# Kernel optimization log

Measured on AMD Instinct MI355X. Metric: run time of the kernel, lower is better.

Reference implementation:

```python
import jax, jax.numpy as jnp
import numpy as np

B = 4
T, Hh, Ww = 16, 32, 32
C = 256
HEADS = 8
WIN = 4
SHIFT = 2
MLP = 1024


def _rel_pos_index(w):
    coords = np.stack(np.meshgrid(np.arange(w), np.arange(w), np.arange(w), indexing='ij')).reshape(3, -1)
    rc = (coords[:, :, None] - coords[:, None, :]).transpose(1, 2, 0)
    rc[:, :, 0] += w - 1
    rc[:, :, 1] += w - 1
    rc[:, :, 2] += w - 1
    rc[:, :, 0] *= (2 * w - 1) * (2 * w - 1)
    rc[:, :, 1] *= 2 * w - 1
    return rc.sum(-1).astype(np.int32)  # (w^3, w^3)


def _attn_mask(t, h, w, win, shift):
    m = np.zeros((t, h, w))
    sl = (slice(0, -win), slice(-win, -shift), slice(-shift, None))
    cnt = 0
    for a in sl:
        for b in sl:
            for c in sl:
                m[a, b, c] = cnt
                cnt += 1
    m = m.reshape(t // win, win, h // win, win, w // win, win).transpose(0, 2, 4, 1, 3, 5).reshape(-1, win ** 3)
    am = m[:, None, :] - m[:, :, None]  # (nW, N, N)
    return np.where(am != 0, -100.0, 0.0).astype(np.float32)


def setup_inputs() -> dict:
    key = jax.random.key(0)
    ks = jax.random.split(key, 12)
    s_in = 1.0 / np.sqrt(C)
    s_mlp = 1.0 / np.sqrt(MLP)
    return {
        'x': jax.random.normal(ks[0], (B, T * Hh * Ww, C), jnp.float32),
        'norm1_g': jnp.ones((C,), jnp.float32),
        'norm1_b': jnp.zeros((C,), jnp.float32),
        'qkv_w': jax.random.normal(ks[1], (C, 3 * C), jnp.float32) * s_in,
        'qkv_b': jax.random.normal(ks[2], (3 * C,), jnp.float32) * 0.02,
        'proj_w': jax.random.normal(ks[3], (C, C), jnp.float32) * s_in,
        'proj_b': jax.random.normal(ks[4], (C,), jnp.float32) * 0.02,
        'rel_bias_table': jax.random.normal(ks[5], ((2 * WIN - 1) ** 3, HEADS), jnp.float32) * 0.02,
        'norm2_g': jnp.ones((C,), jnp.float32),
        'norm2_b': jnp.zeros((C,), jnp.float32),
        'mlp_w1': jax.random.normal(ks[6], (C, MLP), jnp.float32) * s_in,
        'mlp_b1': jax.random.normal(ks[7], (MLP,), jnp.float32) * 0.02,
        'mlp_w2': jax.random.normal(ks[8], (MLP, C), jnp.float32) * s_mlp,
        'mlp_b2': jax.random.normal(ks[9], (C,), jnp.float32) * 0.02,
        'rel_index': jnp.asarray(_rel_pos_index(WIN)),
        'attn_mask': jnp.asarray(_attn_mask(T, Hh, Ww, WIN, SHIFT)),
    }


def _ln(x, g, b, eps):
    mu = x.mean(-1, keepdims=True)
    var = ((x - mu) ** 2).mean(-1, keepdims=True)
    return (x - mu) * jax.lax.rsqrt(var + eps) * g + b


def reference(x, norm1_g, norm1_b, qkv_w, qkv_b, proj_w, proj_b, rel_bias_table,
              norm2_g, norm2_b, mlp_w1, mlp_b1, mlp_w2, mlp_b2, rel_index, attn_mask):
    w = WIN
    N = w ** 3
    hd = C // HEADS
    scale = hd ** -0.5

    h = _ln(x, norm1_g, norm1_b, 1e-5).reshape(B, T, Hh, Ww, C)
    h = jnp.roll(h, shift=(-SHIFT, -SHIFT, -SHIFT), axis=(1, 2, 3))
    # window partition -> (B*nW, N, C)
    h = h.reshape(B, T // w, w, Hh // w, w, Ww // w, w, C)
    h = h.transpose(0, 1, 3, 5, 2, 4, 6, 7).reshape(-1, N, C)

    qkv = (h @ qkv_w + qkv_b).reshape(-1, N, 3, HEADS, hd)
    qkv = qkv.transpose(2, 0, 3, 1, 4)  # (3, BW, heads, N, hd)
    q, k, v = qkv[0] * scale, qkv[1], qkv[2]
    attn = jnp.einsum('bhid,bhjd->bhij', q, k)

    bias = rel_bias_table[rel_index.reshape(-1)].reshape(N, N, HEADS).transpose(2, 0, 1)
    attn = attn + bias[None]

    nW = attn_mask.shape[0]
    attn = attn.reshape(-1, nW, HEADS, N, N) + attn_mask[None, :, None]
    attn = jax.nn.softmax(attn.reshape(-1, HEADS, N, N), axis=-1)

    o = jnp.einsum('bhij,bhjd->bhid', attn, v).transpose(0, 2, 1, 3).reshape(-1, N, C)
    o = o @ proj_w + proj_b
    # window reverse
    o = o.reshape(B, T // w, Hh // w, Ww // w, w, w, w, C)
    o = o.transpose(0, 1, 4, 2, 5, 3, 6, 7).reshape(B, T, Hh, Ww, C)
    o = jnp.roll(o, shift=(SHIFT, SHIFT, SHIFT), axis=(1, 2, 3)).reshape(B, T * Hh * Ww, C)

    x = x + o
    y = _ln(x, norm2_g, norm2_b, 1e-6)
    y = jax.nn.gelu(y @ mlp_w1 + mlp_b1, approximate=False) @ mlp_w2 + mlp_b2
    return x + y
```

## Files before the change

kernel.cpp:

```cpp
#include <hip/hip_runtime.h>
#include <cstdint>
#include <cstddef>

typedef float  f32x4_t  __attribute__((ext_vector_type(4)));
typedef __bf16 bf16x8_t __attribute__((ext_vector_type(8)));
typedef __bf16 bf16x4_t __attribute__((ext_vector_type(4)));

#define NTOK   65536
#define CCH    256
#define NWINT  1024

__device__ __forceinline__ float wred_sum(float v) {
#pragma unroll
  for (int off = 32; off > 0; off >>= 1) v += __shfl_xor(v, off, 64);
  return v;
}

__device__ __forceinline__ void gload16(void* lds, const void* g) {
  __builtin_amdgcn_global_load_lds(
      (const __attribute__((address_space(1))) uint32_t*)g,
      (__attribute__((address_space(3))) uint32_t*)lds, 16, 0, 0);
}

__device__ __forceinline__ int win_to_orig(int token) {
  int gid = token >> 6, n = token & 63;
  int bb = gid >> 8, rem = gid & 255;
  int t = (((rem >> 6) << 2) + (n >> 4) + 2) & 15;
  int h = ((((rem >> 3) & 7) << 2) + ((n >> 2) & 3) + 2) & 31;
  int w = (((rem & 7) << 2) + (n & 3) + 2) & 31;
  return ((bb * 16 + t) * 32 + h) * 32 + w;
}

__global__ __launch_bounds__(256) void prep_weights(
    const float* __restrict__ qkv_w, const float* __restrict__ proj_w,
    const float* __restrict__ mlp_w1, const float* __restrict__ mlp_w2,
    __bf16* __restrict__ wt_qkv, __bf16* __restrict__ wt_proj,
    __bf16* __restrict__ wt_mlp1, __bf16* __restrict__ wt_mlp2) {
  int i = blockIdx.x * 256 + threadIdx.x;
  if (i < 196608) {
    int k = i / 768, n = i % 768;
    wt_qkv[n * 256 + k] = (__bf16)qkv_w[i];
  } else if (i < 262144) {
    int j = i - 196608;
    int k = j >> 8, n = j & 255;
    wt_proj[n * 256 + k] = (__bf16)proj_w[j];
  } else if (i < 524288) {
    int j = i - 262144;
    int k = j >> 10, n = j & 1023;
    wt_mlp1[n * 256 + k] = (__bf16)mlp_w1[j];
  } else {
    int j = i - 524288;
    int k = j >> 8, n = j & 255;
    wt_mlp2[n * 1024 + k] = (__bf16)mlp_w2[j];
  }
}

__global__ __launch_bounds__(256) void cm_prep(
    const float* __restrict__ table, const int* __restrict__ ridx,
    const float* __restrict__ mask, __bf16* __restrict__ cm) {
  int tid = blockIdx.x * 256 + threadIdx.x;
  int l = tid & 63;
  int t16 = (tid >> 6) & 15;
  int h = (tid >> 10) & 7;
  int w = tid >> 13;
  int it = t16 & 3, jt = t16 >> 2;
  int i = it * 16 + (l & 15);
  int jb = jt * 16 + ((l >> 4) << 2);
  const float* mrow = mask + (size_t)w * 4096 + i * 64;
  const int* rrow = ridx + i * 64;
  bf16x4_t o;
#pragma unroll
  for (int r = 0; r < 4; ++r) {
    int j = jb + r;
    o[r] = (__bf16)(table[rrow[j] * 8 + h] + mrow[j]);
  }
  *(bf16x4_t*)(cm + (size_t)tid * 4) = o;
}

template <int MODE>
__global__ __launch_bounds__(256) void ln_kernel(
    const float* __restrict__ xin, const float* __restrict__ g,
    const float* __restrict__ b, __bf16* __restrict__ out, float eps) {
  int token = blockIdx.x * 4 + (threadIdx.x >> 6);
  int lane = threadIdx.x & 63;
  size_t src = (MODE == 0) ? (size_t)win_to_orig(token) : (size_t)token;
  f32x4_t v = ((const f32x4_t*)(xin + src * CCH))[lane];
  float mu = wred_sum(v[0] + v[1] + v[2] + v[3]) * (1.0f / 256.0f);
  float d0 = v[0] - mu, d1 = v[1] - mu, d2 = v[2] - mu, d3 = v[3] - mu;
  float var = wred_sum(d0 * d0 + d1 * d1 + d2 * d2 + d3 * d3) * (1.0f / 256.0f);
  float rs = rsqrtf(var + eps);
  f32x4_t gg = ((const f32x4_t*)g)[lane];
  f32x4_t bb = ((const f32x4_t*)b)[lane];
  bf16x4_t o;
  o[0] = (__bf16)(d0 * rs * gg[0] + bb[0]);
  o[1] = (__bf16)(d1 * rs * gg[1] + bb[1]);
  o[2] = (__bf16)(d2 * rs * gg[2] + bb[2]);
  o[3] = (__bf16)(d3 * rs * gg[3] + bb[3]);
  *(bf16x4_t*)(out + (size_t)token * CCH + lane * 4) = o;
}

#define BM 128
#define BN 128
#define BK 64
template <int EPI>
__global__ __launch_bounds__(256) void gemm_kernel(
    const __bf16* __restrict__ A, const __bf16* __restrict__ Bt,
    const float* __restrict__ bias, const float* __restrict__ res,
    void* __restrict__ outp, int M, int N, int K) {
  __shared__ bf16x8_t smA[1024];
  __shared__ bf16x8_t smB[1024];
  const int wv = threadIdx.x >> 6;
  const int ln = threadIdx.x & 63;
  const int bm = blockIdx.y * BM;
  const int bn = blockIdx.x * BN;
  const int wr = wv >> 1, wc = wv & 1;

  f32x4_t acc[4][4];
#pragma unroll
  for (int m = 0; m < 4; ++m)
#pragma unroll
    for (int n = 0; n < 4; ++n) acc[m][n] = (f32x4_t){0.f, 0.f, 0.f, 0.f};

  const int KT = K >> 6;
  for (int kt = 0; kt < KT; ++kt) {
#pragma unroll
    for (int it = 0; it < 4; ++it) {
      int base = (it * 4 + wv) * 64;
      int slot = base + ln;
      int row = slot >> 3;
      int chunk = (slot & 7) ^ (row & 7);
      gload16((void*)(smA + base),
              (const void*)(A + (size_t)(bm + row) * K + kt * BK + chunk * 8));
      gload16((void*)(smB + base),
              (const void*)(Bt + (size_t)(bn + row) * K + kt * BK + chunk * 8));
    }
    __syncthreads();

#pragma unroll
    for (int kh = 0; kh < 2; ++kh) {
      bf16x8_t af[4], bfr[4];
#pragma unroll
      for (int m = 0; m < 4; ++m) {
        int row = wr * 64 + m * 16 + (ln & 15);
        int c = (kh * 4 + (ln >> 4)) ^ (row & 7);
        af[m] = *(const bf16x8_t*)((const char*)smA + row * 128 + c * 16);
      }
#pragma unroll
      for (int n = 0; n < 4; ++n) {
        int row = wc * 64 + n * 16 + (ln & 15);
        int c = (kh * 4 + (ln >> 4)) ^ (row & 7);
        bfr[n] = *(const bf16x8_t*)((const char*)smB + row * 128 + c * 16);
      }
#pragma unroll
      for (int m = 0; m < 4; ++m)
#pragma unroll
        for (int n = 0; n < 4; ++n)
          acc[m][n] = __builtin_amdgcn_mfma_f32_16x16x32_bf16(
              af[m], bfr[n], acc[m][n], 0, 0, 0);
    }
    __syncthreads();
  }

#pragma unroll
  for (int m = 0; m < 4; ++m) {
    int grow0 = bm + wr * 64 + m * 16 + ((ln >> 4) * 4);
#pragma unroll
    for (int n = 0; n < 4; ++n) {
      int gcol = bn + wc * 64 + n * 16 + (ln & 15);
      float bv = bias[gcol];
#pragma unroll
      for (int r = 0; r < 4; ++r) {
        int grow = grow0 + r;
        float v = acc[m][n][r] + bv;
        if constexpr (EPI == 0) {
          ((__bf16*)outp)[(size_t)grow * N + gcol] = (__bf16)v;
        } else if constexpr (EPI == 1) {
          size_t dst = (size_t)win_to_orig(grow) * CCH + gcol;
          ((float*)outp)[dst] = res[dst] + v;
        } else if constexpr (EPI == 2) {
          float gl = 0.5f * v * (1.0f + erff(v * 0.70710678118654752f));
          ((__bf16*)outp)[(size_t)grow * N + gcol] = (__bf16)gl;
        } else {
          size_t o = (size_t)grow * N + gcol;
          ((float*)outp)[o] = res[o] + v;
        }
      }
    }
  }
}

__global__ __launch_bounds__(256) void attn_mfma(
    const __bf16* __restrict__ qkv, const __bf16* __restrict__ cm,
    __bf16* __restrict__ owin) {
  __shared__ __align__(16) __bf16 smP[4][64 * 72];
  __shared__ __align__(16) __bf16 smV[4][64 * 32];
  const int wv = threadIdx.x >> 6;
  const int ln = threadIdx.x & 63;
  const int task = blockIdx.x * 4 + wv;
  const int win = task >> 3;
  const int h = task & 7;
  const int i15 = ln & 15, g = ln >> 4;

  const __bf16* base = qkv + (size_t)win * 64 * 768 + h * 32;

  {
    __bf16* vdst = smV[wv];
#pragma unroll
    for (int c = 0; c < 4; ++c) {
      const __bf16* src =
          base + (size_t)(c * 16 + (ln >> 2)) * 768 + 512 + (ln & 3) * 8;
      gload16(vdst + c * 512, src);
    }
  }

  bf16x8_t kf[4], qf[4];
#pragma unroll
  for (int t = 0; t < 4; ++t) {
    kf[t] = *(const bf16x8_t*)(base + (size_t)(t * 16 + i15) * 768 + 256 + g * 8);
    qf[t] = *(const bf16x8_t*)(base + (size_t)(t * 16 + i15) * 768 + g * 8);
  }

  f32x4_t st[4][4];
#pragma unroll
  for (int jt = 0; jt < 4; ++jt)
#pragma unroll
    for (int it = 0; it < 4; ++it)
      st[jt][it] = __builtin_amdgcn_mfma_f32_16x16x32_bf16(
          kf[jt], qf[it], (f32x4_t){0.f, 0.f, 0.f, 0.f}, 0, 0, 0);

  const __bf16* cmp = cm + (((size_t)(win & 255) * 8 + h) * 16) * 256;
#pragma unroll
  for (int jt = 0; jt < 4; ++jt)
#pragma unroll
    for (int it = 0; it < 4; ++it) {
      bf16x4_t c4 = *(const bf16x4_t*)(cmp + ((jt * 4 + it) * 64 + ln) * 4);
#pragma unroll
      for (int r = 0; r < 4; ++r)
        st[jt][it][r] =
            fmaf(st[jt][it][r], 0.17677669529663687f, (float)c4[r]);
    }

#pragma unroll
  for (int it = 0; it < 4; ++it) {
    float mx = -1e30f;
#pragma unroll
    for (int jt = 0; jt < 4; ++jt)
#pragma unroll
      for (int r = 0; r < 4; ++r) mx = fmaxf(mx, st[jt][it][r]);
    mx = fmaxf(mx, __shfl_xor(mx, 16, 64));
    mx = fmaxf(mx, __shfl_xor(mx, 32, 64));
    float sum = 0.f;
#pragma unroll
    for (int jt = 0; jt < 4; ++jt)
#pragma unroll
      for (int r = 0; r < 4; ++r) {
        float p = __expf(st[jt][it][r] - mx);
        st[jt][it][r] = p;
        sum += p;
      }
    sum += __shfl_xor(sum, 16, 64);
    sum += __shfl_xor(sum, 32, 64);
    float inv = 1.0f / sum;
#pragma unroll
    for (int jt = 0; jt < 4; ++jt) {
      bf16x4_t p4;
#pragma unroll
      for (int r = 0; r < 4; ++r) p4[r] = (__bf16)(st[jt][it][r] * inv);
      *(bf16x4_t*)(smP[wv] + (it * 16 + i15) * 72 + jt * 16 + g * 4) = p4;
    }
  }
  __syncthreads();

  f32x4_t oacc[4][2];
#pragma unroll
  for (int it = 0; it < 4; ++it)
#pragma unroll
    for (int dt = 0; dt < 2; ++dt) oacc[it][dt] = (f32x4_t){0.f, 0.f, 0.f, 0.f};

  const __bf16* pl = smP[wv];
  const __bf16* vl = smV[wv];
#pragma unroll
  for (int kt = 0; kt < 2; ++kt) {
    bf16x8_t vf[2];
#pragma unroll
    for (int dt = 0; dt < 2; ++dt)
#pragma unroll
      for (int e = 0; e < 8; ++e)
        vf[dt][e] = vl[(kt * 32 + g * 8 + e) * 32 + dt * 16 + i15];
#pragma unroll
    for (int it = 0; it < 4; ++it) {
      bf16x8_t pa =
          *(const bf16x8_t*)(pl + (it * 16 + i15) * 72 + kt * 32 + g * 8);
#pragma unroll
      for (int dt = 0; dt < 2; ++dt)
        oacc[it][dt] = __builtin_amdgcn_mfma_f32_16x16x32_bf16(
            pa, vf[dt], oacc[it][dt], 0, 0, 0);
    }
  }

  __bf16* op = owin + (size_t)win * 64 * 256 + h * 32;
#pragma unroll
  for (int it = 0; it < 4; ++it)
#pragma unroll
    for (int r = 0; r < 4; ++r) {
      int i = it * 16 + g * 4 + r;
#pragma unroll
      for (int dt = 0; dt < 2; ++dt)
        op[(size_t)i * 256 + dt * 16 + i15] = (__bf16)oacc[it][dt][r];
    }
}

extern "C" void kernel_launch(void* const* d_in, const int* in_sizes, int n_in,
                              void* d_out, int out_size, void* d_ws,
                              size_t ws_size, hipStream_t stream) {
  (void)in_sizes; (void)n_in; (void)out_size; (void)ws_size;
  const float* x      = (const float*)d_in[0];
  const float* n1g    = (const float*)d_in[1];
  const float* n1b    = (const float*)d_in[2];
  const float* qkv_w  = (const float*)d_in[3];
  const float* qkv_b  = (const float*)d_in[4];
  const float* proj_w = (const float*)d_in[5];
  const float* proj_b = (const float*)d_in[6];
  const float* rbt    = (const float*)d_in[7];
  const float* n2g    = (const float*)d_in[8];
  const float* n2b    = (const float*)d_in[9];
  const float* mlp_w1 = (const float*)d_in[10];
  const float* mlp_b1 = (const float*)d_in[11];
  const float* mlp_w2 = (const float*)d_in[12];
  const float* mlp_b2 = (const float*)d_in[13];
  const int*   ridx   = (const int*)d_in[14];
  const float* amask  = (const float*)d_in[15];

  char* ws = (char*)d_ws;
  size_t off = 0;
  auto alloc = [&](size_t bytes) {
    void* p = ws + off;
    off += (bytes + 255) & ~(size_t)255;
    return p;
  };
  __bf16* wt_qkv  = (__bf16*)alloc(768 * 256 * 2);
  __bf16* wt_proj = (__bf16*)alloc(256 * 256 * 2);
  __bf16* wt_mlp1 = (__bf16*)alloc(1024 * 256 * 2);
  __bf16* wt_mlp2 = (__bf16*)alloc(1024 * 256 * 2);
  __bf16* hwin = (__bf16*)alloc((size_t)NTOK * 256 * 2);
  __bf16* qkv  = (__bf16*)alloc((size_t)NTOK * 768 * 2);
  __bf16* owin = (__bf16*)alloc((size_t)NTOK * 256 * 2);
  __bf16* cmb  = hwin;
  __bf16* yb   = hwin;
  __bf16* mlph = qkv;
  float* x2    = (float*)d_out;

  prep_weights<<<3072, 256, 0, stream>>>(qkv_w, proj_w, mlp_w1, mlp_w2,
                                         wt_qkv, wt_proj, wt_mlp1, wt_mlp2);
  ln_kernel<0><<<NTOK / 4, 256, 0, stream>>>(x, n1g, n1b, hwin, 1e-5f);
  gemm_kernel<0><<<dim3(768 / BN, NTOK / BM), 256, 0, stream>>>(
      hwin, wt_qkv, qkv_b, nullptr, qkv, NTOK, 768, 256);
  cm_prep<<<8192, 256, 0, stream>>>(rbt, ridx, amask, cmb);
  attn_mfma<<<2048, 256, 0, stream>>>(qkv, cmb, owin);
  gemm_kernel<1><<<dim3(256 / BN, NTOK / BM), 256, 0, stream>>>(
      owin, wt_proj, proj_b, x, x2, NTOK, 256, 256);
  ln_kernel<1><<<NTOK / 4, 256, 0, stream>>>(x2, n2g, n2b, yb, 1e-6f);
  gemm_kernel<2><<<dim3(1024 / BN, NTOK / BM), 256, 0, stream>>>(
      yb, wt_mlp1, mlp_b1, nullptr, mlph, NTOK, 1024, 256);
  gemm_kernel<3><<<dim3(256 / BN, NTOK / BM), 256, 0, stream>>>(
      mlph, wt_mlp2, mlp_b2, x2, d_out, NTOK, 256, 1024);
}
```

Baseline: 361.9 us.

## Double-buffer GEMM LDS tiles with async prefetch and XCD-aware block remap

The GEMM kernel now keeps two LDS buffers for the A and B tiles. It issues the next k-tile's global-to-LDS loads before computing on the current one, using explicit vmcnt waits and barriers, so memory latency overlaps with MFMA work. The 2D grid becomes 1D, and block ids are remapped round-robin across the 8 XCDs for better L2 locality. Pointer increments replace per-iteration address math, and the epilogue hoists the bias loads and the win_to_orig row mapping. LDS use doubles, which may lower occupancy, and the hand-written waitcnt counts must match the issued loads exactly.

Result: no change. 359.8 us (-0.6%).

```diff
diff --git a/kernel.cpp b/kernel.cpp
--- a/kernel.cpp
+++ b/kernel.cpp
@@ -107,14 +107,30 @@
     const __bf16* __restrict__ A, const __bf16* __restrict__ Bt,
     const float* __restrict__ bias, const float* __restrict__ res,
     void* __restrict__ outp, int M, int N, int K) {
-  __shared__ bf16x8_t smA[1024];
-  __shared__ bf16x8_t smB[1024];
+  __shared__ __bf16 smA[2][8192];
+  __shared__ __bf16 smB[2][8192];
   const int wv = threadIdx.x >> 6;
   const int ln = threadIdx.x & 63;
-  const int bm = blockIdx.y * BM;
-  const int bn = blockIdx.x * BN;
+  const int i15 = ln & 15, g = ln >> 4;
+
+  int nwg = gridDim.x;
+  int wgid = ((int)blockIdx.x & 7) * (nwg >> 3) + ((int)blockIdx.x >> 3);
+  int nx = N >> 7;
+  int bx = wgid % nx, by = wgid / nx;
+  const int bm = by * BM, bn = bx * BN;
   const int wr = wv >> 1, wc = wv & 1;
 
+  const __bf16* aP[4];
+  const __bf16* bP[4];
+#pragma unroll
+  for (int it = 0; it < 4; ++it) {
+    int slot = (it * 4 + wv) * 64 + ln;
+    int row = slot >> 3;
+    int chunk = (slot & 7) ^ (row & 7);
+    aP[it] = A + (size_t)(bm + row) * K + chunk * 8;
+    bP[it] = Bt + (size_t)(bn + row) * K + chunk * 8;
+  }
+
   f32x4_t acc[4][4];
 #pragma unroll
   for (int m = 0; m < 4; ++m)
@@ -122,35 +138,31 @@
     for (int n = 0; n < 4; ++n) acc[m][n] = (f32x4_t){0.f, 0.f, 0.f, 0.f};
 
   const int KT = K >> 6;
-  for (int kt = 0; kt < KT; ++kt) {
+
+  auto stage = [&](int buf) {
 #pragma unroll
     for (int it = 0; it < 4; ++it) {
-      int base = (it * 4 + wv) * 64;
-      int slot = base + ln;
-      int row = slot >> 3;
-      int chunk = (slot & 7) ^ (row & 7);
-      gload16((void*)(smA + base),
-              (const void*)(A + (size_t)(bm + row) * K + kt * BK + chunk * 8));
-      gload16((void*)(smB + base),
-              (const void*)(Bt + (size_t)(bn + row) * K + kt * BK + chunk * 8));
-    }
-    __syncthreads();
-
+      int base = (it * 4 + wv) * 512;
+      gload16(&smA[buf][base], aP[it]);
+      gload16(&smB[buf][base], bP[it]);
+      aP[it] += BK;
+      bP[it] += BK;
+    }
+  };
+
+  auto compute = [&](int buf) {
+    const __bf16* lA = smA[buf];
+    const __bf16* lB = smB[buf];
 #pragma unroll
     for (int kh = 0; kh < 2; ++kh) {
+      int cA = (((kh * 4) + g) ^ (i15 & 7)) * 8;
       bf16x8_t af[4], bfr[4];
 #pragma unroll
-      for (int m = 0; m < 4; ++m) {
-        int row = wr * 64 + m * 16 + (ln & 15);
-        int c = (kh * 4 + (ln >> 4)) ^ (row & 7);
-        af[m] = *(const bf16x8_t*)((const char*)smA + row * 128 + c * 16);
-      }
-#pragma unroll
-      for (int n = 0; n < 4; ++n) {
-        int row = wc * 64 + n * 16 + (ln & 15);
-        int c = (kh * 4 + (ln >> 4)) ^ (row & 7);
-        bfr[n] = *(const bf16x8_t*)((const char*)smB + row * 128 + c * 16);
-      }
+      for (int m = 0; m < 4; ++m)
+        af[m] = *(const bf16x8_t*)(lA + (wr * 64 + m * 16 + i15) * 64 + cA);
+#pragma unroll
+      for (int n = 0; n < 4; ++n)
+        bfr[n] = *(const bf16x8_t*)(lB + (wc * 64 + n * 16 + i15) * 64 + cA);
 #pragma unroll
       for (int m = 0; m < 4; ++m)
 #pragma unroll
@@ -158,30 +170,51 @@
           acc[m][n] = __builtin_amdgcn_mfma_f32_16x16x32_bf16(
               af[m], bfr[n], acc[m][n], 0, 0, 0);
     }
-    __syncthreads();
-  }
-
+  };
+
+  stage(0);
+  for (int kt = 0; kt < KT - 1; ++kt) {
+    stage((kt + 1) & 1);
+    asm volatile("s_waitcnt vmcnt(8)" ::: "memory");
+    __builtin_amdgcn_s_barrier();
+    asm volatile("" ::: "memory");
+    compute(kt & 1);
+    asm volatile("s_waitcnt lgkmcnt(0)" ::: "memory");
+    __builtin_amdgcn_s_barrier();
+  }
+  asm volatile("s_waitcnt vmcnt(0)" ::: "memory");
+  __builtin_amdgcn_s_barrier();
+  asm volatile("" ::: "memory");
+  compute((KT - 1) & 1);
+
+  float bv[4];
+#pragma unroll
+  for (int n = 0; n < 4; ++n) bv[n] = bias[bn + wc * 64 + n * 16 + i15];
 #pragma unroll
   for (int m = 0; m < 4; ++m) {
-    int grow0 = bm + wr * 64 + m * 16 + ((ln >> 4) * 4);
-#pragma unroll
-    for (int n = 0; n < 4; ++n) {
-      int gcol = bn + wc * 64 + n * 16 + (ln & 15);
-      float bv = bias[gcol];
-#pragma unroll
-      for (int r = 0; r < 4; ++r) {
-        int grow = grow0 + r;
-        float v = acc[m][n][r] + bv;
+    int grow0 = bm + wr * 64 + m * 16 + g * 4;
+#pragma unroll
+    for (int r = 0; r < 4; ++r) {
+      int grow = grow0 + r;
+      size_t rowbase;
+      if constexpr (EPI == 1)
+        rowbase = (size_t)win_to_orig(grow) * CCH;
+      else
+        rowbase = (size_t)grow * N;
+#pragma unroll
+      for (int n = 0; n < 4; ++n) {
+        int gcol = bn + wc * 64 + n * 16 + i15;
+        float v = acc[m][n][r] + bv[n];
         if constexpr (EPI == 0) {
-          ((__bf16*)outp)[(size_t)grow * N + gcol] = (__bf16)v;
+          ((__bf16*)outp)[rowbase + gcol] = (__bf16)v;
         } else if constexpr (EPI == 1) {
-          size_t dst = (size_t)win_to_orig(grow) * CCH + gcol;
+          size_t dst = rowbase + gcol;
           ((float*)outp)[dst] = res[dst] + v;
         } else if constexpr (EPI == 2) {
           float gl = 0.5f * v * (1.0f + erff(v * 0.70710678118654752f));
-          ((__bf16*)outp)[(size_t)grow * N + gcol] = (__bf16)gl;
+          ((__bf16*)outp)[rowbase + gcol] = (__bf16)gl;
         } else {
-          size_t o = (size_t)grow * N + gcol;
+          size_t o = rowbase + gcol;
           ((float*)outp)[o] = res[o] + v;
         }
       }
@@ -353,15 +386,15 @@
   prep_weights<<<3072, 256, 0, stream>>>(qkv_w, proj_w, mlp_w1, mlp_w2,
                                          wt_qkv, wt_proj, wt_mlp1, wt_mlp2);
   ln_kernel<0><<<NTOK / 4, 256, 0, stream>>>(x, n1g, n1b, hwin, 1e-5f);
-  gemm_kernel<0><<<dim3(768 / BN, NTOK / BM), 256, 0, stream>>>(
+  gemm_kernel<0><<<(768 / BN) * (NTOK / BM), 256, 0, stream>>>(
       hwin, wt_qkv, qkv_b, nullptr, qkv, NTOK, 768, 256);
   cm_prep<<<8192, 256, 0, stream>>>(rbt, ridx, amask, cmb);
   attn_mfma<<<2048, 256, 0, stream>>>(qkv, cmb, owin);
-  gemm_kernel<1><<<dim3(256 / BN, NTOK / BM), 256, 0, stream>>>(
+  gemm_kernel<1><<<(256 / BN) * (NTOK / BM), 256, 0, stream>>>(
       owin, wt_proj, proj_b, x, x2, NTOK, 256, 256);
   ln_kernel<1><<<NTOK / 4, 256, 0, stream>>>(x2, n2g, n2b, yb, 1e-6f);
-  gemm_kernel<2><<<dim3(1024 / BN, NTOK / BM), 256, 0, stream>>>(
+  gemm_kernel<2><<<(1024 / BN) * (NTOK / BM), 256, 0, stream>>>(
       yb, wt_mlp1, mlp_b1, nullptr, mlph, NTOK, 1024, 256);
-  gemm_kernel<3><<<dim3(256 / BN, NTOK / BM), 256, 0, stream>>>(
+  gemm_kernel<3><<<(256 / BN) * (NTOK / BM), 256, 0, stream>>>(
       mlph, wt_mlp2, mlp_b2, x2, d_out, NTOK, 256, 1024);
 }
```

## Rewrite GEMMs with double-buffered 64x256 tiles and fuse proj with LayerNorm2

Applied to the files above, without the earlier changes.

Replaces the generic 128x128 GEMM with a templated 64x256-tile kernel that double-buffers the K loop in LDS with BK=32, uses workgroup-id swizzling and vectorized epilogue stores. Fuses the projection GEMM, the residual add and the second LayerNorm into one kernel that computes row statistics through LDS, which removes a separate LN pass over x2. Swaps the erf GELU for a tanh-approximation built on exp, which is cheaper but approximate. The MLP stage now stores h1 and yb in original token order instead of window order. Larger tiles and the launch bound of 4 may raise register pressure.

Result: faster. 350.7 us (-3.1%).

```diff
diff --git a/kernel.cpp b/kernel.cpp
--- a/kernel.cpp
+++ b/kernel.cpp
@@ -8,7 +8,6 @@
 
 #define NTOK   65536
 #define CCH    256
-#define NWINT  1024
 
 __device__ __forceinline__ float wred_sum(float v) {
 #pragma unroll
@@ -29,6 +28,12 @@
   int h = ((((rem >> 3) & 7) << 2) + ((n >> 2) & 3) + 2) & 31;
   int w = (((rem & 7) << 2) + (n & 3) + 2) & 31;
   return ((bb * 16 + t) * 32 + h) * 32 + w;
+}
+
+__device__ __forceinline__ float gelu_f(float v) {
+  float u = v * (0.7978845608028654f + 0.03567740814f * v * v);
+  float t = 1.0f - 2.0f / (__expf(2.0f * u) + 1.0f);
+  return 0.5f * v * (1.0f + t);
 }
 
 __global__ __launch_bounds__(256) void prep_weights(
@@ -77,13 +82,12 @@
   *(bf16x4_t*)(cm + (size_t)tid * 4) = o;
 }
 
-template <int MODE>
 __global__ __launch_bounds__(256) void ln_kernel(
     const float* __restrict__ xin, const float* __restrict__ g,
     const float* __restrict__ b, __bf16* __restrict__ out, float eps) {
   int token = blockIdx.x * 4 + (threadIdx.x >> 6);
   int lane = threadIdx.x & 63;
-  size_t src = (MODE == 0) ? (size_t)win_to_orig(token) : (size_t)token;
+  size_t src = (size_t)win_to_orig(token);
   f32x4_t v = ((const f32x4_t*)(xin + src * CCH))[lane];
   float mu = wred_sum(v[0] + v[1] + v[2] + v[3]) * (1.0f / 256.0f);
   float d0 = v[0] - mu, d1 = v[1] - mu, d2 = v[2] - mu, d3 = v[3] - mu;
@@ -99,92 +103,212 @@
   *(bf16x4_t*)(out + (size_t)token * CCH + lane * 4) = o;
 }
 
-#define BM 128
-#define BN 128
-#define BK 64
-template <int EPI>
-__global__ __launch_bounds__(256) void gemm_kernel(
+
+#define GEMM_KLOOP(KT)                                                        \
+  stage(0, 0);                                                                \
+  asm volatile("s_waitcnt vmcnt(0)" ::: "memory");                            \
+  __syncthreads();                                                            \
+  _Pragma("unroll") for (int kt = 0; kt < (KT); ++kt) {                       \
+    const int cur = kt & 1;                                                   \
+    if (kt + 1 < (KT)) stage(cur ^ 1, kt + 1);                                \
+    const __bf16* lA = smA[cur];                                              \
+    const __bf16* lB = smB[cur];                                              \
+    bf16x8_t af[4], wf[4];                                                    \
+    _Pragma("unroll") for (int mm = 0; mm < 4; ++mm)                          \
+        af[mm] = *(const bf16x8_t*)((const char*)lA + (mm * 16 + i15) * 64 +  \
+                                    (((g ^ (i15 & 3))) << 4));                \
+    _Pragma("unroll") for (int nn = 0; nn < 4; ++nn)                          \
+        wf[nn] = *(const bf16x8_t*)((const char*)lB +                         \
+                                    (wv * 64 + nn * 16 + i15) * 64 +          \
+                                    (((g ^ (i15 & 3))) << 4));                \
+    _Pragma("unroll") for (int nn = 0; nn < 4; ++nn)                          \
+        _Pragma("unroll") for (int mm = 0; mm < 4; ++mm)                      \
+            acc[nn][mm] = __builtin_amdgcn_mfma_f32_16x16x32_bf16(            \
+                wf[nn], af[mm], acc[nn][mm], 0, 0, 0);                        \
+    if (kt + 1 < (KT)) {                                                      \
+      asm volatile("s_waitcnt vmcnt(0) lgkmcnt(0)" ::: "memory");             \
+      __syncthreads();                                                        \
+    }                                                                         \
+  }
+
+template <int N, int K, int EPI>
+__global__ __launch_bounds__(256, 4) void gemm_c(
     const __bf16* __restrict__ A, const __bf16* __restrict__ Bt,
     const float* __restrict__ bias, const float* __restrict__ res,
-    void* __restrict__ outp, int M, int N, int K) {
-  __shared__ bf16x8_t smA[1024];
-  __shared__ bf16x8_t smB[1024];
-  const int wv = threadIdx.x >> 6;
-  const int ln = threadIdx.x & 63;
-  const int bm = blockIdx.y * BM;
-  const int bn = blockIdx.x * BN;
-  const int wr = wv >> 1, wc = wv & 1;
+    void* __restrict__ outp) {
+  constexpr int KT = K / 32;
+  constexpr int NX = N / 256;
+  __shared__ __bf16 smA[2][64 * 32];
+  __shared__ __bf16 smB[2][256 * 32];
+  const int tid = threadIdx.x;
+  const int wv = tid >> 6, ln = tid & 63;
+  const int i15 = ln & 15, g = ln >> 4;
+
+  int nwg = gridDim.x;
+  int wgid = ((int)blockIdx.x & 7) * (nwg >> 3) + ((int)blockIdx.x >> 3);
+  const int bx = wgid % NX, by = wgid / NX;
+  const int bm = by * 64, bn = bx * 256;
+
+  const int rowA = tid >> 2, chA = (tid & 3) ^ ((tid >> 2) & 3);
+  const __bf16* aP = A + (size_t)(bm + rowA) * K + chA * 8;
+  const __bf16* bP[4];
+#pragma unroll
+  for (int rnd = 0; rnd < 4; ++rnd) {
+    int slot = rnd * 256 + tid;
+    int row = slot >> 2, ch = (slot & 3) ^ (row & 3);
+    bP[rnd] = Bt + (size_t)(bn + row) * K + ch * 8;
+  }
+
+  auto stage = [&](int buf, int kt) {
+    gload16(&smA[buf][wv * 512], aP + kt * 32);
+#pragma unroll
+    for (int rnd = 0; rnd < 4; ++rnd)
+      gload16(&smB[buf][rnd * 2048 + wv * 512], bP[rnd] + kt * 32);
+  };
 
   f32x4_t acc[4][4];
 #pragma unroll
-  for (int m = 0; m < 4; ++m)
-#pragma unroll
-    for (int n = 0; n < 4; ++n) acc[m][n] = (f32x4_t){0.f, 0.f, 0.f, 0.f};
-
-  const int KT = K >> 6;
-  for (int kt = 0; kt < KT; ++kt) {
-#pragma unroll
-    for (int it = 0; it < 4; ++it) {
-      int base = (it * 4 + wv) * 64;
-      int slot = base + ln;
-      int row = slot >> 3;
-      int chunk = (slot & 7) ^ (row & 7);
-      gload16((void*)(smA + base),
-              (const void*)(A + (size_t)(bm + row) * K + kt * BK + chunk * 8));
-      gload16((void*)(smB + base),
-              (const void*)(Bt + (size_t)(bn + row) * K + kt * BK + chunk * 8));
-    }
-    __syncthreads();
-
-#pragma unroll
-    for (int kh = 0; kh < 2; ++kh) {
-      bf16x8_t af[4], bfr[4];
-#pragma unroll
-      for (int m = 0; m < 4; ++m) {
-        int row = wr * 64 + m * 16 + (ln & 15);
-        int c = (kh * 4 + (ln >> 4)) ^ (row & 7);
-        af[m] = *(const bf16x8_t*)((const char*)smA + row * 128 + c * 16);
+  for (int nn = 0; nn < 4; ++nn)
+#pragma unroll
+    for (int mm = 0; mm < 4; ++mm) acc[nn][mm] = (f32x4_t){0.f, 0.f, 0.f, 0.f};
+
+  GEMM_KLOOP(KT)
+
+#pragma unroll
+  for (int nn = 0; nn < 4; ++nn) {
+    int colg = bn + wv * 64 + nn * 16 + g * 4;
+    f32x4_t bv = *(const f32x4_t*)(bias + colg);
+#pragma unroll
+    for (int mm = 0; mm < 4; ++mm) {
+      int rowg = bm + mm * 16 + i15;
+      if constexpr (EPI == 0) {
+        bf16x4_t o;
+#pragma unroll
+        for (int r = 0; r < 4; ++r) o[r] = (__bf16)(acc[nn][mm][r] + bv[r]);
+        *(bf16x4_t*)((__bf16*)outp + (size_t)rowg * N + colg) = o;
+      } else if constexpr (EPI == 1) {
+        bf16x4_t o;
+#pragma unroll
+        for (int r = 0; r < 4; ++r)
+          o[r] = (__bf16)gelu_f(acc[nn][mm][r] + bv[r]);
+        *(bf16x4_t*)((__bf16*)outp + (size_t)rowg * N + colg) = o;
+      } else {
+        size_t off = (size_t)rowg * N + colg;
+        f32x4_t rv = *(const f32x4_t*)(res + off);
+        f32x4_t o;
+#pragma unroll
+        for (int r = 0; r < 4; ++r) o[r] = rv[r] + acc[nn][mm][r] + bv[r];
+        *(f32x4_t*)((float*)outp + off) = o;
       }
-#pragma unroll
-      for (int n = 0; n < 4; ++n) {
-        int row = wc * 64 + n * 16 + (ln & 15);
-        int c = (kh * 4 + (ln >> 4)) ^ (row & 7);
-        bfr[n] = *(const bf16x8_t*)((const char*)smB + row * 128 + c * 16);
+    }
+  }
+}
+
+__global__ __launch_bounds__(256, 4) void proj_ln(
+    const __bf16* __restrict__ A, const __bf16* __restrict__ Bt,
+    const float* __restrict__ bias, const float* __restrict__ res,
+    const float* __restrict__ g2, const float* __restrict__ b2,
+    float* __restrict__ x2, __bf16* __restrict__ yb) {
+  constexpr int K = 256, KT = 8;
+  __shared__ __bf16 smA[2][64 * 32];
+  __shared__ __bf16 smB[2][256 * 32];
+  __shared__ float2 stf[256];
+  const int tid = threadIdx.x;
+  const int wv = tid >> 6, ln = tid & 63;
+  const int i15 = ln & 15, g = ln >> 4;
+
+  int nwg = gridDim.x;
+  int wgid = ((int)blockIdx.x & 7) * (nwg >> 3) + ((int)blockIdx.x >> 3);
+  const int bm = wgid * 64;
+
+  const int rowA = tid >> 2, chA = (tid & 3) ^ ((tid >> 2) & 3);
+  const __bf16* aP = A + (size_t)(bm + rowA) * K + chA * 8;
+  const __bf16* bP[4];
+#pragma unroll
+  for (int rnd = 0; rnd < 4; ++rnd) {
+    int slot = rnd * 256 + tid;
+    int row = slot >> 2, ch = (slot & 3) ^ (row & 3);
+    bP[rnd] = Bt + (size_t)row * K + ch * 8;
+  }
+
+  auto stage = [&](int buf, int kt) {
+    gload16(&smA[buf][wv * 512], aP + kt * 32);
+#pragma unroll
+    for (int rnd = 0; rnd < 4; ++rnd)
+      gload16(&smB[buf][rnd * 2048 + wv * 512], bP[rnd] + kt * 32);
+  };
+
+  f32x4_t acc[4][4];
+#pragma unroll
+  for (int nn = 0; nn < 4; ++nn)
+#pragma unroll
+    for (int mm = 0; mm < 4; ++mm) acc[nn][mm] = (f32x4_t){0.f, 0.f, 0.f, 0.f};
+
+  GEMM_KLOOP(KT)
+
+  size_t dst[4];
+#pragma unroll
+  for (int mm = 0; mm < 4; ++mm)
+    dst[mm] = (size_t)win_to_orig(bm + mm * 16 + i15) * CCH;
+#pragma unroll
+  for (int nn = 0; nn < 4; ++nn) {
+    int colg = wv * 64 + nn * 16 + g * 4;
+    f32x4_t bv = *(const f32x4_t*)(bias + colg);
+#pragma unroll
+    for (int mm = 0; mm < 4; ++mm) {
+      f32x4_t rv = *(const f32x4_t*)(res + dst[mm] + colg);
+#pragma unroll
+      for (int r = 0; r < 4; ++r) acc[nn][mm][r] += bv[r] + rv[r];
+    }
+  }
+
+#pragma unroll
+  for (int mm = 0; mm < 4; ++mm) {
+    float s1 = 0.f, s2 = 0.f;
+#pragma unroll
+    for (int nn = 0; nn < 4; ++nn)
+#pragma unroll
+      for (int r = 0; r < 4; ++r) {
+        float v = acc[nn][mm][r];
+        s1 += v;
+        s2 += v * v;
       }
-#pragma unroll
-      for (int m = 0; m < 4; ++m)
-#pragma unroll
-        for (int n = 0; n < 4; ++n)
-          acc[m][n] = __builtin_amdgcn_mfma_f32_16x16x32_bf16(
-              af[m], bfr[n], acc[m][n], 0, 0, 0);
-    }
-    __syncthreads();
-  }
-
-#pragma unroll
-  for (int m = 0; m < 4; ++m) {
-    int grow0 = bm + wr * 64 + m * 16 + ((ln >> 4) * 4);
-#pragma unroll
-    for (int n = 0; n < 4; ++n) {
-      int gcol = bn + wc * 64 + n * 16 + (ln & 15);
-      float bv = bias[gcol];
-#pragma unroll
-      for (int r = 0; r < 4; ++r) {
-        int grow = grow0 + r;
-        float v = acc[m][n][r] + bv;
-        if constexpr (EPI == 0) {
-          ((__bf16*)outp)[(size_t)grow * N + gcol] = (__bf16)v;
-        } else if constexpr (EPI == 1) {
-          size_t dst = (size_t)win_to_orig(grow) * CCH + gcol;
-          ((float*)outp)[dst] = res[dst] + v;
-        } else if constexpr (EPI == 2) {
-          float gl = 0.5f * v * (1.0f + erff(v * 0.70710678118654752f));
-          ((__bf16*)outp)[(size_t)grow * N + gcol] = (__bf16)gl;
-        } else {
-          size_t o = (size_t)grow * N + gcol;
-          ((float*)outp)[o] = res[o] + v;
-        }
-      }
+    s1 += __shfl_xor(s1, 16, 64);
+    s1 += __shfl_xor(s1, 32, 64);
+    s2 += __shfl_xor(s2, 16, 64);
+    s2 += __shfl_xor(s2, 32, 64);
+    if (g == 0) stf[(mm * 16 + i15) * 4 + wv] = make_float2(s1, s2);
+  }
+  __syncthreads();
+  float mu[4], rs[4];
+#pragma unroll
+  for (int mm = 0; mm < 4; ++mm) {
+    int row = mm * 16 + i15;
+    float S1 = 0.f, S2 = 0.f;
+#pragma unroll
+    for (int w = 0; w < 4; ++w) {
+      float2 p = stf[row * 4 + w];
+      S1 += p.x;
+      S2 += p.y;
+    }
+    mu[mm] = S1 * (1.0f / 256.0f);
+    rs[mm] = rsqrtf(S2 * (1.0f / 256.0f) - mu[mm] * mu[mm] + 1e-6f);
+  }
+
+#pragma unroll
+  for (int nn = 0; nn < 4; ++nn) {
+    int colg = wv * 64 + nn * 16 + g * 4;
+    f32x4_t gv = *(const f32x4_t*)(g2 + colg);
+    f32x4_t bv = *(const f32x4_t*)(b2 + colg);
+#pragma unroll
+    for (int mm = 0; mm < 4; ++mm) {
+      f32x4_t v = acc[nn][mm];
+      *(f32x4_t*)(x2 + dst[mm] + colg) = v;
+      bf16x4_t yo;
+#pragma unroll
+      for (int r = 0; r < 4; ++r)
+        yo[r] = (__bf16)((v[r] - mu[mm]) * rs[mm] * gv[r] + bv[r]);
+      *(bf16x4_t*)(yb + dst[mm] + colg) = yo;
     }
   }
 }
@@ -347,21 +471,20 @@
   __bf16* owin = (__bf16*)alloc((size_t)NTOK * 256 * 2);
   __bf16* cmb  = hwin;
   __bf16* yb   = hwin;
-  __bf16* mlph = qkv;
+  __bf16* h1   = qkv;
   float* x2    = (float*)d_out;
 
   prep_weights<<<3072, 256, 0, stream>>>(qkv_w, proj_w, mlp_w1, mlp_w2,
                                          wt_qkv, wt_proj, wt_mlp1, wt_mlp2);
-  ln_kernel<0><<<NTOK / 4, 256, 0, stream>>>(x, n1g, n1b, hwin, 1e-5f);
-  gemm_kernel<0><<<dim3(768 / BN, NTOK / BM), 256, 0, stream>>>(
-      hwin, wt_qkv, qkv_b, nullptr, qkv, NTOK, 768, 256);
+  ln_kernel<<<NTOK / 4, 256, 0, stream>>>(x, n1g, n1b, hwin, 1e-5f);
+  gemm_c<768, 256, 0><<<3 * (NTOK / 64), 256, 0, stream>>>(
+      hwin, wt_qkv, qkv_b, nullptr, qkv);
   cm_prep<<<8192, 256, 0, stream>>>(rbt, ridx, amask, cmb);
   attn_mfma<<<2048, 256, 0, stream>>>(qkv, cmb, owin);
-  gemm_kernel<1><<<dim3(256 / BN, NTOK / BM), 256, 0, stream>>>(
-      owin, wt_proj, proj_b, x, x2, NTOK, 256, 256);
-  ln_kernel<1><<<NTOK / 4, 256, 0, stream>>>(x2, n2g, n2b, yb, 1e-6f);
-  gemm_kernel<2><<<dim3(1024 / BN, NTOK / BM), 256, 0, stream>>>(
-      yb, wt_mlp1, mlp_b1, nullptr, mlph, NTOK, 1024, 256);
-  gemm_kernel<3><<<dim3(256 / BN, NTOK / BM), 256, 0, stream>>>(
-      mlph, wt_mlp2, mlp_b2, x2, d_out, NTOK, 256, 1024);
-}
+  proj_ln<<<NTOK / 64, 256, 0, stream>>>(owin, wt_proj, proj_b, x, n2g, n2b,
+                                         x2, yb);
+  gemm_c<1024, 256, 1><<<4 * (NTOK / 64), 256, 0, stream>>>(
+      yb, wt_mlp1, mlp_b1, nullptr, h1);
+  gemm_c<256, 1024, 2><<<NTOK / 64, 256, 0, stream>>>(
+      h1, wt_mlp2, mlp_b2, x2, d_out);
+}
```
